# Performance work log

Hardware: AMD Instinct MI355X
Metric: run time of the kernel (lower is better)

Reference implementation:

```python
import jax, jax.numpy as jnp
import numpy as np


def setup_inputs() -> dict:
    key = jax.random.key(0)
    k1, k2 = jax.random.split(key)
    n_rows, cols, n_values = 4096, 2048, 16
    x = jax.random.normal(k1, (n_rows, cols), dtype=jnp.float32)
    values = jax.random.normal(k2, (n_rows, n_values), dtype=jnp.float32)
    return {"x": x, "values": values}


def reference(x, values):
    # x: [R, C], values: [R, V] (per-row codebook)
    # distances: [R, C, V] broadcast squared distance
    distances = (x[:, :, None] - values[:, None, :]) ** 2
    min_indices = jnp.argmin(distances, axis=-1)          # [R, C]
    # gather nearest codebook value per row
    selected = jnp.take_along_axis(values, min_indices, axis=1)  # [R, C]
    return selected
```

## Files before the change

kernel.cpp:

```cpp
#include <hip/hip_runtime.h>
#include <math.h>


#define N_ROWS 4096
#define N_COLS 2048
#define N_VALS 16

typedef float f32x4 __attribute__((ext_vector_type(4)));

__device__ __forceinline__ unsigned ford(unsigned u) {
    return (u & 0x80000000u) ? ~u : (u | 0x80000000u);
}
__device__ __forceinline__ unsigned funord(unsigned o) {
    return (o & 0x80000000u) ? (o & 0x7fffffffu) : ~o;
}

__global__ __launch_bounds__(256) void vq_rowcodebook_kernel(
    const float* __restrict__ x,
    const float* __restrict__ values,
    float* __restrict__ out)
{
    const int row = blockIdx.x;
    const float* vr = values + (size_t)row * N_VALS;
    const int tid = threadIdx.x;

    __shared__ float LUT[32];
    __shared__ int   SIDX[16];

    if (tid < N_VALS) {
        const float vi = vr[tid];
        int rank = 0;
#pragma unroll
        for (int j = 0; j < N_VALS; ++j) {
            const float vj = vr[j];
            rank += (vj < vi || (vj == vi && j < tid)) ? 1 : 0;
        }
        LUT[16 + rank] = vi;
        SIDX[rank] = tid;
        if (tid == 0) LUT[0] = -INFINITY;
    }
    __syncthreads();

    if (tid >= 1 && tid < N_VALS) {
        const float a = LUT[16 + tid - 1];
        const float b = LUT[16 + tid];
        const int  ia = SIDX[tid - 1];
        const int  ib = SIDX[tid];
        unsigned L = ford(__float_as_uint(a));
        unsigned H = ford(__float_as_uint(b)) + 1u;
        while (L < H) {
            const unsigned M = L + ((H - L) >> 1);
            const float xm = __uint_as_float(funord(M));
            const float tL = xm - a;
            const float tR = xm - b;
            const float dL = tL * tL;
            const float dR = tR * tR;
            const bool takeR = (dR < dL) || ((dR == dL) && (ib < ia));
            if (takeR) H = M; else L = M + 1;
        }
        LUT[tid] = __uint_as_float(funord(L));
    }
    __syncthreads();

    const float t8  = LUT[8];
    const float t4  = LUT[4];
    const float t12 = LUT[12];
    const char* base = (const char*)LUT;

    const f32x4* xr   = (const f32x4*)(x   + (size_t)row * N_COLS);
    f32x4*       outr = (f32x4*)      (out + (size_t)row * N_COLS);

#pragma unroll
    for (int it = 0; it < 2; ++it) {
        const int j = tid + it * 256;
        const f32x4 xv = xr[j];

        f32x4 o;
#pragma unroll
        for (int e = 0; e < 4; ++e) {
            const float xe = xv[e];

            const bool b1 = (t8 <= xe);
            int posB = b1 ? 32 : 0;
            const float tq = b1 ? t12 : t4;
            posB += (tq <= xe) ? 16 : 0;
            posB += (*(const float*)(base + posB + 8) <= xe) ? 8 : 0;
            posB += (*(const float*)(base + posB + 4) <= xe) ? 4 : 0;

            o[e] = *(const float*)(base + posB + 64);
        }
        outr[j] = o;
    }
}

extern "C" void kernel_launch(void* const* d_in, const int* in_sizes, int n_in,
                              void* d_out, int out_size, void* d_ws, size_t ws_size,
                              hipStream_t stream) {
    const float* x      = (const float*)d_in[0];
    const float* values = (const float*)d_in[1];
    float* out          = (float*)d_out;

    vq_rowcodebook_kernel<<<N_ROWS, 256, 0, stream>>>(x, values, out);
}
```

Before: 86.51 us.

## Process two rows per block and prefetch x before codebook threshold setup

Each block now handles two rows, and all x vectors for both rows are loaded into registers before the per-row sort and binary-search threshold computation. The global load latency therefore overlaps the serial setup phase instead of waiting behind the syncthreads barriers, and the setup cost is shared across twice the work. The binary search also starts one step tighter and uses a precomputed tie flag. In exchange the block count is halved and register pressure rises from holding four float4 values across the barriers.

```diff
diff --git a/kernel.cpp b/kernel.cpp
--- a/kernel.cpp
+++ b/kernel.cpp
@@ -5,6 +5,7 @@
 #define N_ROWS 4096
 #define N_COLS 2048
 #define N_VALS 16
+#define ROWS_PER_BLOCK 2
 
 typedef float f32x4 __attribute__((ext_vector_type(4)));
 
@@ -20,76 +21,82 @@
     const float* __restrict__ values,
     float* __restrict__ out)
 {
-    const int row = blockIdx.x;
-    const float* vr = values + (size_t)row * N_VALS;
+    const int row0 = blockIdx.x * ROWS_PER_BLOCK;
     const int tid = threadIdx.x;
 
-    __shared__ float LUT[32];
-    __shared__ int   SIDX[16];
+    __shared__ float LUT[ROWS_PER_BLOCK][32];
+    __shared__ int   SIDX[ROWS_PER_BLOCK][16];
 
-    if (tid < N_VALS) {
-        const float vi = vr[tid];
+    const f32x4* xr0 = (const f32x4*)(x + (size_t)row0 * N_COLS);
+    f32x4 xv0 = xr0[tid];
+    f32x4 xv1 = xr0[256 + tid];
+    f32x4 xv2 = xr0[512 + tid];
+    f32x4 xv3 = xr0[768 + tid];
+
+    if (tid < ROWS_PER_BLOCK * N_VALS) {
+        const int rr = tid >> 4, i = tid & 15;
+        const float* vr = values + (size_t)(row0 + rr) * N_VALS;
+        const float vi = vr[i];
         int rank = 0;
 #pragma unroll
         for (int j = 0; j < N_VALS; ++j) {
             const float vj = vr[j];
-            rank += (vj < vi || (vj == vi && j < tid)) ? 1 : 0;
+            rank += (vj < vi || (vj == vi && j < i)) ? 1 : 0;
         }
-        LUT[16 + rank] = vi;
-        SIDX[rank] = tid;
-        if (tid == 0) LUT[0] = -INFINITY;
+        LUT[rr][16 + rank] = vi;
+        SIDX[rr][rank] = i;
     }
     __syncthreads();
 
-    if (tid >= 1 && tid < N_VALS) {
-        const float a = LUT[16 + tid - 1];
-        const float b = LUT[16 + tid];
-        const int  ia = SIDX[tid - 1];
-        const int  ib = SIDX[tid];
-        unsigned L = ford(__float_as_uint(a));
-        unsigned H = ford(__float_as_uint(b)) + 1u;
-        while (L < H) {
-            const unsigned M = L + ((H - L) >> 1);
-            const float xm = __uint_as_float(funord(M));
-            const float tL = xm - a;
-            const float tR = xm - b;
-            const float dL = tL * tL;
-            const float dR = tR * tR;
-            const bool takeR = (dR < dL) || ((dR == dL) && (ib < ia));
-            if (takeR) H = M; else L = M + 1;
+    if (tid < ROWS_PER_BLOCK * N_VALS) {
+        const int rr = tid >> 4, i = tid & 15;
+        if (i >= 1) {
+            const float a = LUT[rr][16 + i - 1];
+            const float b = LUT[rr][16 + i];
+            const bool tiewin = (SIDX[rr][i] < SIDX[rr][i - 1]);
+            unsigned L = ford(__float_as_uint(a)) + 1u;
+            unsigned H = ford(__float_as_uint(b)) + 1u;
+            while (L < H) {
+                const unsigned M = L + ((H - L) >> 1);
+                const float xm = __uint_as_float(funord(M));
+                const float tL = xm - a;
+                const float tR = xm - b;
+                const float dL = tL * tL;
+                const float dR = tR * tR;
+                const bool takeR = (dR == dL) ? tiewin : (dR < dL);
+                if (takeR) H = M; else L = M + 1;
+            }
+            LUT[rr][i] = __uint_as_float(funord(L));
         }
-        LUT[tid] = __uint_as_float(funord(L));
     }
     __syncthreads();
 
-    const float t8  = LUT[8];
-    const float t4  = LUT[4];
-    const float t12 = LUT[12];
-    const char* base = (const char*)LUT;
-
-    const f32x4* xr   = (const f32x4*)(x   + (size_t)row * N_COLS);
-    f32x4*       outr = (f32x4*)      (out + (size_t)row * N_COLS);
+#pragma unroll
+    for (int rr = 0; rr < ROWS_PER_BLOCK; ++rr) {
+        const char* base = (const char*)&LUT[rr][0];
+        const float t4  = LUT[rr][4];
+        const float t8  = LUT[rr][8];
+        const float t12 = LUT[rr][12];
+        f32x4* outr = (f32x4*)(out + (size_t)(row0 + rr) * N_COLS);
 
 #pragma unroll
-    for (int it = 0; it < 2; ++it) {
-        const int j = tid + it * 256;
-        const f32x4 xv = xr[j];
-
-        f32x4 o;
+        for (int it = 0; it < 2; ++it) {
+            const f32x4 v = (rr == 0) ? (it == 0 ? xv0 : xv1)
+                                      : (it == 0 ? xv2 : xv3);
+            f32x4 o;
 #pragma unroll
-        for (int e = 0; e < 4; ++e) {
-            const float xe = xv[e];
-
-            const bool b1 = (t8 <= xe);
-            int posB = b1 ? 32 : 0;
-            const float tq = b1 ? t12 : t4;
-            posB += (tq <= xe) ? 16 : 0;
-            posB += (*(const float*)(base + posB + 8) <= xe) ? 8 : 0;
-            posB += (*(const float*)(base + posB + 4) <= xe) ? 4 : 0;
-
-            o[e] = *(const float*)(base + posB + 64);
+            for (int e = 0; e < 4; ++e) {
+                const float xe = v[e];
+                const bool b1 = (t8 <= xe);
+                int posB = b1 ? 32 : 0;
+                const float tq = b1 ? t12 : t4;
+                posB += (tq <= xe) ? 16 : 0;
+                posB += (*(const float*)(base + posB + 8) <= xe) ? 8 : 0;
+                posB += (*(const float*)(base + posB + 4) <= xe) ? 4 : 0;
+                o[e] = *(const float*)(base + posB + 64);
+            }
+            outr[it * 256 + tid] = o;
         }
-        outr[j] = o;
     }
 }
 
@@ -100,5 +107,5 @@
     const float* values = (const float*)d_in[1];
     float* out          = (float*)d_out;
 
-    vq_rowcodebook_kernel<<<N_ROWS, 256, 0, stream>>>(x, values, out);
+    vq_rowcodebook_kernel<<<N_ROWS / ROWS_PER_BLOCK, 256, 0, stream>>>(x, values, out);
 }
```

Measured after the change: 85.20 us. About the same (-1.5%).
